# Optimization experiments

Measured on AMD Instinct MI355X. Metric: run time of the kernel, lower is better.

Reference implementation:

```python
import jax, jax.numpy as jnp
import numpy as np
from jax import lax

B, C, D, NH, H, W = 32, 768, 512, 4, 24, 24
HD = C // NH          # 192
FHW = H * W           # 576 (must equal 24*24 per o_proj_img2)


def _p(key, shape, scale=0.02):
    return scale * jax.random.normal(key, shape, dtype=jnp.float32)


def setup_inputs() -> dict:
    ks = jax.random.split(jax.random.key(0), 10)
    return dict(
        img_feats=jax.random.normal(ks[0], (B, C, H, W), jnp.float32),
        txt_feats=jax.random.normal(ks[1], (B, D), jnp.float32),
        fn_w=jnp.ones((C,), jnp.float32), fn_b=jnp.zeros((C,), jnp.float32),
        gn_w=jnp.ones((D,), jnp.float32), gn_b=jnp.zeros((D,), jnp.float32),
        qkv_img_w=_p(ks[2], (3 * C, C)),
        qkv_txt_w=_p(ks[3], (3 * C, D)),
        o_img_w=_p(ks[4], (C, C)), o_img_b=jnp.zeros((C,), jnp.float32),
        o_img2_w=_p(ks[5], (FHW, HD)), o_img2_b=jnp.zeros((FHW,), jnp.float32),
        ffn_norm_w=jnp.ones((C,), jnp.float32), ffn_norm_b=jnp.zeros((C,), jnp.float32),
        fc1_w=_p(ks[6], (C, C)),
        dw_w=_p(ks[7], (C, 1, 3, 3)),
        fc2_w=_p(ks[8], (C, C)),
    )


def layernorm2d(x, w, b, eps=1e-6):
    # normalize over channel dim (dim 1) of NCHW
    u = x.mean(1, keepdims=True)
    s = ((x - u) ** 2).mean(1, keepdims=True)
    x = (x - u) * lax.rsqrt(s + eps)
    return w[:, None, None] * x + b[:, None, None]


def l2norm_last(x, eps=1e-12):
    # F.normalize(x, dim=-1): divide by L2 norm clamped at eps
    n = jnp.sqrt(jnp.sum(x * x, axis=-1, keepdims=True))
    return x / jnp.maximum(n, eps)


def _forward(img_feats, txt_feats, fn_w, fn_b, gn_w, gn_b, qkv_img_w, qkv_txt_w,
             o_img_w, o_img_b, o_img2_w, o_img2_b, ffn_norm_w, ffn_norm_b,
             fc1_w, dw_w, fc2_w):
    x = layernorm2d(img_feats, fn_w, fn_b)
    # guide LayerNorm (torch default eps=1e-5, biased var)
    mu = txt_feats.mean(-1, keepdims=True)
    var = jnp.mean((txt_feats - mu) ** 2, axis=-1, keepdims=True)
    t = (txt_feats - mu) * lax.rsqrt(var + 1e-5) * gn_w + gn_b

    # qkv img: 1x1 conv; channel layout (ng nh hd) -> [B,3,NH,HD,F]
    qkv_img = jnp.einsum('bchw,oc->bohw', x, qkv_img_w).reshape(B, 3, NH, HD, FHW)
    q_img, k_img, v_img = qkv_img[:, 0], qkv_img[:, 1], qkv_img[:, 2]

    # qkv txt: layout 'b (nh (ng hd))' per the two rearranges -> [B,NH,3,HD]
    qkv_txt = (t @ qkv_txt_w.T).reshape(B, NH, 3, HD)
    q_txt, k_txt = qkv_txt[:, :, 0], qkv_txt[:, :, 1]

    # normalize over size-1 trailing dim == x / max(|x|, eps)  (sign-like)
    nq_txt = q_txt / jnp.maximum(jnp.abs(q_txt), 1e-12)          # [B,NH,HD]
    nk_img = l2norm_last(k_img)                                  # [B,NH,HD,F]
    # einsum('bnhd,bnhf->bnhf') with d of size 1 == broadcast multiply over h
    attn1 = jax.nn.softmax(nq_txt[..., None] * nk_img, axis=-1)  # [B,NH,HD,F]
    txt_on_img = jnp.einsum('bnhf,bngf->bnhg', attn1, v_img)     # [B,NH,HD,HD]

    nk_txt = k_txt / jnp.maximum(jnp.abs(k_txt), 1e-12)
    nq_img = l2norm_last(q_img)
    attn2 = jax.nn.softmax(nk_txt[..., None] * nq_img, axis=-1)
    txt_to_img2 = jnp.einsum('bnhf,bngf->bnhg', attn2, v_img)

    img = (txt_on_img + txt_to_img2).reshape(B, NH * HD, HD)     # [B,768,192]
    y = (img @ o_img2_w.T + o_img2_b).reshape(B, C, H, W)        # [B,768,24,24]
    out = jnp.einsum('bchw,oc->bohw', y, o_img_w) + o_img_b[None, :, None, None] + img_feats

    # ConvMlp FFN (mlp_times=1, bias=False convs, exact GELU)
    z = layernorm2d(out, ffn_norm_w, ffn_norm_b)
    z = jnp.einsum('bchw,oc->bohw', z, fc1_w)
    z = lax.conv_general_dilated(z, dw_w, (1, 1), 'SAME',
                                 feature_group_count=C,
                                 dimension_numbers=('NCHW', 'OIHW', 'NCHW'))
    z = jax.nn.gelu(z, approximate=False)
    z = jnp.einsum('bchw,oc->bohw', z, fc2_w)
    return out + z


def reference(img_feats, txt_feats, fn_w, fn_b, gn_w, gn_b, qkv_img_w, qkv_txt_w,
              o_img_w, o_img_b, o_img2_w, o_img2_b, ffn_norm_w, ffn_norm_b,
              fc1_w, dw_w, fc2_w):
    return _forward(img_feats, txt_feats, fn_w, fn_b, gn_w, gn_b, qkv_img_w,
                    qkv_txt_w, o_img_w, o_img_b, o_img2_w, o_img2_b,
                    ffn_norm_w, ffn_norm_b, fc1_w, dw_w, fc2_w)
```

## Files before the change

kernel.cpp:

```cpp
#include <hip/hip_runtime.h>

typedef unsigned short u16;
typedef __attribute__((ext_vector_type(8))) short short8_t;
typedef __attribute__((ext_vector_type(4))) float f32x4;
typedef __attribute__((ext_vector_type(4))) unsigned short u16x4;

static constexpr int cB   = 32;
static constexpr int cC   = 768;
static constexpr int cD   = 512;
static constexpr int cNH  = 4;
static constexpr int cHD  = 192;
static constexpr int cFHW = 576;
static constexpr int cC3  = 2304;

__device__ inline float us2f(u16 s) {
    union { unsigned int u; float f; } v; v.u = ((unsigned int)s) << 16; return v.f;
}
__device__ inline u16 f2bf(float f) {
    union { float f; unsigned int u; } v; v.f = f;
    unsigned int r = v.u + 0x7FFFu + ((v.u >> 16) & 1u);
    return (u16)(r >> 16);
}
__device__ inline float ldflex(const void* p, size_t i, int isf32) {
    return isf32 ? ((const float*)p)[i] : us2f(((const u16*)p)[i]);
}

__device__ inline void gload16(const void* g, void* l) {
    __builtin_amdgcn_global_load_lds(
        (const __attribute__((address_space(1))) void*)g,
        (__attribute__((address_space(3))) void*)l, 16, 0, 0);
}

__global__ void detect_kernel(const u16* __restrict__ raw, int* __restrict__ flags) {
    flags[0] = (raw[0] == 0x3F80u) ? 0 : 1;
}

struct FlatDesc { const void* src[12]; float* dst[12]; int off[13]; };
__global__ __launch_bounds__(256) void flatten_kernel(FlatDesc d, const int* __restrict__ flags) {
    const int isf = flags[0];
    const int gid = blockIdx.x * 256 + threadIdx.x;
    if (gid >= d.off[12]) return;
    int s = 0;
    #pragma unroll
    for (int i = 1; i < 12; i++) s += (gid >= d.off[i]) ? 1 : 0;
    const int j = gid - d.off[s];
    d.dst[s][j] = ldflex(d.src[s], j, isf);
}

__global__ __launch_bounds__(256) void cast_bf16_kernel(
    const void* __restrict__ src, u16* __restrict__ dst, int n, const int* __restrict__ flags)
{
    const int isf = flags[0];
    for (int i = blockIdx.x * 256 + threadIdx.x; i < n; i += gridDim.x * 256)
        dst[i] = isf ? f2bf(((const float*)src)[i]) : ((const u16*)src)[i];
}

__global__ __launch_bounds__(256) void transpose_kernel(
    const void* __restrict__ src, float* __restrict__ dst,
    int Mdim, int Kdim, const int* __restrict__ flags)
{
    __shared__ float t[32][33];
    const int isf = flags[0];
    const int k0 = blockIdx.x * 32, m0 = blockIdx.y * 32;
    const int x = threadIdx.x & 31, y = threadIdx.x >> 5;
    #pragma unroll
    for (int i = 0; i < 4; i++) {
        const int m = y + i * 8;
        t[m][x] = ldflex(src, (size_t)(m0 + m) * Kdim + k0 + x, isf);
    }
    __syncthreads();
    #pragma unroll
    for (int i = 0; i < 4; i++) {
        const int r = y + i * 8;
        dst[(size_t)(k0 + r) * Mdim + m0 + x] = t[x][r];
    }
}

__global__ __launch_bounds__(256) void txt_ln_kernel(
    const float* __restrict__ txt, const float* __restrict__ gw, const float* __restrict__ gb,
    float* __restrict__ tln)
{
    __shared__ float red[8];
    const int b = blockIdx.x, tid = threadIdx.x;
    const float v0 = txt[(size_t)b * cD + tid];
    const float v1 = txt[(size_t)b * cD + 256 + tid];
    float s = v0 + v1, ss = v0 * v0 + v1 * v1;
    #pragma unroll
    for (int o = 1; o < 64; o <<= 1) { s += __shfl_xor(s, o, 64); ss += __shfl_xor(ss, o, 64); }
    const int wid = tid >> 6, lane = tid & 63;
    if (lane == 0) { red[wid] = s; red[4 + wid] = ss; }
    __syncthreads();
    s  = red[0] + red[1] + red[2] + red[3];
    ss = red[4] + red[5] + red[6] + red[7];
    const float mean = s * (1.f / cD);
    const float var  = fmaxf(ss * (1.f / cD) - mean * mean, 0.f);
    const float r = rsqrtf(var + 1e-5f);
    tln[(size_t)b * cD + tid]       = (v0 - mean) * r * gw[tid]       + gb[tid];
    tln[(size_t)b * cD + 256 + tid] = (v1 - mean) * r * gw[tid + 256] + gb[tid + 256];
}

__global__ __launch_bounds__(256) void txt_gemm_kernel(
    const float* __restrict__ Wt, const float* __restrict__ tln, float* __restrict__ out)
{
    const int o  = blockIdx.x * 256 + threadIdx.x;
    const int b0 = blockIdx.y * 8;
    __shared__ float t[8][cD];
    for (int i = threadIdx.x; i < 8 * cD; i += 256)
        t[i >> 9][i & (cD - 1)] = tln[(size_t)(b0 + (i >> 9)) * cD + (i & (cD - 1))];
    __syncthreads();
    float acc[8] = {};
    #pragma unroll 2
    for (int k = 0; k < cD; k += 4) {
        const float w0 = Wt[(size_t)(k + 0) * cC3 + o];
        const float w1 = Wt[(size_t)(k + 1) * cC3 + o];
        const float w2 = Wt[(size_t)(k + 2) * cC3 + o];
        const float w3 = Wt[(size_t)(k + 3) * cC3 + o];
        #pragma unroll
        for (int b = 0; b < 8; b++) {
            const float4 tv = *(const float4*)&t[b][k];
            acc[b] += w0 * tv.x + w1 * tv.y + w2 * tv.z + w3 * tv.w;
        }
    }
    #pragma unroll
    for (int b = 0; b < 8; b++) out[(size_t)(b0 + b) * cC3 + o] = acc[b];
}

template <int RAW>
__global__ __launch_bounds__(1024) void ln_stats_kernel(
    const void* __restrict__ x, size_t xoff, float* __restrict__ mr,
    const int* __restrict__ flags)
{
    const int isf = RAW ? flags[0] : 1;
    const int b = blockIdx.y;
    const int l = threadIdx.x & 63;
    const int f = (blockIdx.x << 6) + l;
    const int cg = threadIdx.x >> 6;
    const size_t base = (size_t)b * cC * cFHW + f;
    const size_t rbase = RAW ? (xoff + base) : base;
    float s = 0.f, ss = 0.f;
    for (int c = cg; c < cC; c += 16) {
        float v = RAW ? ldflex(x, rbase + (size_t)c * cFHW, isf)
                      : ((const float*)x)[base + (size_t)c * cFHW];
        s += v; ss += v * v;
    }
    __shared__ float S[16][64], SS[16][64];
    S[cg][l] = s; SS[cg][l] = ss;
    __syncthreads();
    if (threadIdx.x < 64) {
        float su = 0.f, sq = 0.f;
        #pragma unroll
        for (int i = 0; i < 16; i++) { su += S[i][l]; sq += SS[i][l]; }
        const float mean = su * (1.f / cC);
        const float var  = fmaxf(sq * (1.f / cC) - mean * mean, 0.f);
        float* o = mr + ((size_t)b * cFHW + f) * 2;
        o[0] = mean; o[1] = rsqrtf(var + 1e-6f);
    }
}

template <int XSRC>
__global__ __launch_bounds__(256) void prep_xt_kernel(
    const void* __restrict__ X, size_t xoff, u16* __restrict__ Xt,
    const float* __restrict__ mr, const float* __restrict__ lnw, const float* __restrict__ lnb,
    const int* __restrict__ flags)
{
    __shared__ float t[64][33];
    const int isf = (XSRC == 2) ? flags[0] : 1;
    const int f0 = blockIdx.x * 32, c0 = blockIdx.y * 64, b = blockIdx.z;
    const int tid = threadIdx.x;
    const int fx = tid & 31, cy = tid >> 5;
    const size_t base = (size_t)b * cC * cFHW;
    #pragma unroll
    for (int i = 0; i < 8; i++) {
        const int c = c0 + cy + i * 8;
        const size_t ei = base + (size_t)c * cFHW + f0 + fx;
        t[cy + i * 8][fx] = (XSRC == 2) ? ldflex(X, xoff + ei, isf) : ((const float*)X)[ei];
    }
    __syncthreads();
    const int cx = tid & 31, fy = tid >> 5;
    #pragma unroll
    for (int i = 0; i < 4; i++) {
        const int fl = fy + i * 8;
        const int f = f0 + fl;
        float v0 = t[cx * 2][fl], v1 = t[cx * 2 + 1][fl];
        if (XSRC >= 1) {
            const float* mp = mr + ((size_t)b * cFHW + f) * 2;
            const float mean = mp[0], rst = mp[1];
            v0 = (v0 - mean) * rst * lnw[c0 + cx * 2]     + lnb[c0 + cx * 2];
            v1 = (v1 - mean) * rst * lnw[c0 + cx * 2 + 1] + lnb[c0 + cx * 2 + 1];
        }
        const unsigned int pk = (unsigned int)f2bf(v0) | ((unsigned int)f2bf(v1) << 16);
        *(unsigned int*)(Xt + base + (size_t)f * cC + c0 + cx * 2) = pk;
    }
}

template <int EPI>
__global__ __launch_bounds__(256, 2) void conv_mfma(
    const u16* __restrict__ Wb, const u16* __restrict__ Xt,
    float* __restrict__ outp, const float* __restrict__ bias_m,
    const void* __restrict__ resRaw, size_t resOff, const float* __restrict__ resF,
    u16* __restrict__ vout,
    int M, int K, int Mt, const int* __restrict__ flags)
{
    const int nwg = 9 * Mt;
    int wg = blockIdx.x;
    {
        const int q = nwg >> 3, r = nwg & 7, x = wg & 7, idx = wg >> 3;
        wg = (x < r ? x * (q + 1) : r * (q + 1) + (x - r) * q) + idx;
    }
    const int xt = wg / Mt, yt = wg - xt * Mt;
    const int n0 = xt * 64, m0 = yt * 256, b = blockIdx.z;

    __shared__ __align__(16) u16 A_s[2][256 * 64];
    __shared__ __align__(16) u16 B_s[2][64 * 64];

    const int tid = threadIdx.x;
    const int w = tid >> 6, lane = tid & 63, lq = lane >> 4, lr = lane & 15;
    const int l8 = lane >> 3, c8 = lane & 7;
    const int xch = ((c8 ^ l8) << 4);

    const u16* wbase = Wb + (size_t)m0 * K;
    const u16* xbase = Xt + ((size_t)b * cFHW + n0) * K;

    f32x4 acc[4][4];
    #pragma unroll
    for (int i = 0; i < 4; i++)
        #pragma unroll
        for (int j = 0; j < 4; j++)
            acc[i][j] = (f32x4)0.f;

    const int nt = K >> 6;

    #pragma unroll
    for (int j = 0; j < 8; ++j) {
        const int r = w * 64 + j * 8 + l8;
        gload16((const char*)(wbase + (size_t)r * K) + xch, (char*)&A_s[0][(w * 64 + j * 8) * 64]);
    }
    #pragma unroll
    for (int j = 0; j < 2; ++j) {
        const int r = w * 16 + j * 8 + l8;
        gload16((const char*)(xbase + (size_t)r * K) + xch, (char*)&B_s[0][(w * 16 + j * 8) * 64]);
    }

    int buf = 0;
    #pragma unroll 1
    for (int t = 0; t < nt; ++t) {
        if (t + 1 < nt) {
            const int k0 = (t + 1) << 6;
            #pragma unroll
            for (int j = 0; j < 8; ++j) {
                const int r = w * 64 + j * 8 + l8;
                gload16((const char*)(wbase + (size_t)r * K + k0) + xch,
                        (char*)&A_s[buf ^ 1][(w * 64 + j * 8) * 64]);
            }
            #pragma unroll
            for (int j = 0; j < 2; ++j) {
                const int r = w * 16 + j * 8 + l8;
                gload16((const char*)(xbase + (size_t)r * K + k0) + xch,
                        (char*)&B_s[buf ^ 1][(w * 16 + j * 8) * 64]);
            }
            asm volatile("s_waitcnt vmcnt(10)" ::: "memory");
        } else {
            asm volatile("s_waitcnt vmcnt(0)" ::: "memory");
        }
        __builtin_amdgcn_s_barrier();
        __builtin_amdgcn_sched_barrier(0);
        __builtin_amdgcn_s_setprio(1);
        const u16* As = &A_s[buf][0];
        const u16* Bs = &B_s[buf][0];
        #pragma unroll
        for (int kk = 0; kk < 2; kk++) {
            short8_t af[4], bfr[4];
            #pragma unroll
            for (int fm = 0; fm < 4; fm++) {
                const int ml = w * 64 + fm * 16 + lr;
                af[fm] = *(const short8_t*)((const char*)As + ml * 128 + ((kk * 64 + lq * 16) ^ ((lr & 7) << 4)));
            }
            #pragma unroll
            for (int fn = 0; fn < 4; fn++) {
                const int nl = fn * 16 + lr;
                bfr[fn] = *(const short8_t*)((const char*)Bs + nl * 128 + ((kk * 64 + lq * 16) ^ ((lr & 7) << 4)));
            }
            #pragma unroll
            for (int fm = 0; fm < 4; fm++)
                #pragma unroll
                for (int fn = 0; fn < 4; fn++)
                    acc[fm][fn] = __builtin_amdgcn_mfma_f32_16x16x32_bf16(af[fm], bfr[fn], acc[fm][fn], 0, 0, 0);
        }
        __builtin_amdgcn_s_setprio(0);
        __builtin_amdgcn_s_barrier();
        buf ^= 1;
    }

    const int isf = (EPI == 1) ? flags[0] : 1;
    (void)isf;
    if constexpr (EPI == 3) {
        if (m0 >= 2 * cC) {
            const int mb = m0 - 2 * cC + w * 64;
            #pragma unroll
            for (int fm = 0; fm < 4; fm++)
                #pragma unroll
                for (int fn = 0; fn < 4; fn++)
                    #pragma unroll
                    for (int i = 0; i < 4; i++) {
                        const int mm = mb + fm * 16 + lq * 4 + i;
                        vout[((size_t)b * cC + mm) * cFHW + n0 + fn * 16 + lr] = f2bf(acc[fm][fn][i]);
                    }
        } else {
            #pragma unroll
            for (int fm = 0; fm < 4; fm++)
                #pragma unroll
                for (int fn = 0; fn < 4; fn++)
                    #pragma unroll
                    for (int i = 0; i < 4; i++) {
                        const int mm = m0 + w * 64 + fm * 16 + lq * 4 + i;
                        outp[((size_t)b * 2 * cC + mm) * cFHW + n0 + fn * 16 + lr] = acc[fm][fn][i];
                    }
        }
        return;
    }
    #pragma unroll
    for (int fm = 0; fm < 4; fm++) {
        #pragma unroll
        for (int fn = 0; fn < 4; fn++) {
            #pragma unroll
            for (int i = 0; i < 4; i++) {
                const int mm = m0 + w * 64 + fm * 16 + lq * 4 + i;
                const size_t o = ((size_t)b * M + mm) * cFHW + n0 + fn * 16 + lr;
                float vv = acc[fm][fn][i];
                if constexpr (EPI == 1) {
                    vv += bias_m[mm] + ldflex(resRaw, resOff + o, isf);
                } else if constexpr (EPI == 2) {
                    vv += resF[o];
                }
                outp[o] = vv;
            }
        }
    }
}

__global__ __launch_bounds__(64) void attn_p_kernel(
    const float* __restrict__ qk, const float* __restrict__ tq, u16* __restrict__ Pbf)
{
    const int idx = blockIdx.x;
    const int h = idx % cHD;
    const int bn = idx / cHD;
    const int n = bn & 3, b = bn >> 2;
    const int lane = threadIdx.x;
    const float* qrow = qk + ((size_t)b * 2 * cC + n * cHD + h) * cFHW;
    const float* krow = qk + ((size_t)b * 2 * cC + cC + n * cHD + h) * cFHW;
    float kvr[9], qvr[9];
    #pragma unroll
    for (int j = 0; j < 9; j++) {
        kvr[j] = krow[lane + j * 64];
        qvr[j] = qrow[lane + j * 64];
    }
    float ssk = 0.f, mink = 3.0e38f, maxk = -3.0e38f;
    float ssq = 0.f, minq = 3.0e38f, maxq = -3.0e38f;
    #pragma unroll
    for (int j = 0; j < 9; j++) {
        const float kv = kvr[j]; ssk += kv * kv; maxk = fmaxf(maxk, kv); mink = fminf(mink, kv);
        const float qv = qvr[j]; ssq += qv * qv; maxq = fmaxf(maxq, qv); minq = fminf(minq, qv);
    }
    #pragma unroll
    for (int o = 1; o < 64; o <<= 1) {
        ssk += __shfl_xor(ssk, o, 64); ssq += __shfl_xor(ssq, o, 64);
        maxk = fmaxf(maxk, __shfl_xor(maxk, o, 64)); mink = fminf(mink, __shfl_xor(mink, o, 64));
        maxq = fmaxf(maxq, __shfl_xor(maxq, o, 64)); minq = fminf(minq, __shfl_xor(minq, o, 64));
    }
    const float qt = tq[(size_t)b * cC3 + n * 3 * cHD + h];
    const float kt = tq[(size_t)b * cC3 + n * 3 * cHD + cHD + h];
    const float sign1 = qt / fmaxf(fabsf(qt), 1e-12f);
    const float sign2 = kt / fmaxf(fabsf(kt), 1e-12f);
    const float a1 = sign1 / fmaxf(sqrtf(ssk), 1e-12f);
    const float a2 = sign2 / fmaxf(sqrtf(ssq), 1e-12f);
    const float m1 = fmaxf(a1 * maxk, a1 * mink);
    const float m2 = fmaxf(a2 * maxq, a2 * minq);
    float e1[9], e2[9];
    float z1 = 0.f, z2 = 0.f;
    #pragma unroll
    for (int j = 0; j < 9; j++) {
        e1[j] = expf(a1 * kvr[j] - m1); z1 += e1[j];
        e2[j] = expf(a2 * qvr[j] - m2); z2 += e2[j];
    }
    #pragma unroll
    for (int o = 1; o < 64; o <<= 1) { z1 += __shfl_xor(z1, o, 64); z2 += __shfl_xor(z2, o, 64); }
    const float iz1 = 1.f / z1, iz2 = 1.f / z2;
    u16* prow = Pbf + ((size_t)b * cC + n * cHD + h) * cFHW;
    #pragma unroll
    for (int j = 0; j < 9; j++)
        prow[lane + j * 64] = f2bf(e1[j] * iz1 + e2[j] * iz2);
}

__global__ __launch_bounds__(256, 2) void pv_mfma(
    const u16* __restrict__ P, const u16* __restrict__ V, u16* __restrict__ img, int nbn)
{
    const int nwg = 3 * nbn;
    int wg = blockIdx.x;
    {
        const int q = nwg >> 3, r = nwg & 7, x = wg & 7, idx = wg >> 3;
        wg = (x < r ? x * (q + 1) : r * (q + 1) + (x - r) * q) + idx;
    }
    const int bn = wg / 3, gt = wg - bn * 3;
    const int g0 = gt * 64;
    const int b = bn >> 2, n = bn & 3;

    __shared__ __align__(16) u16 A_s[2][192 * 64];
    __shared__ __align__(16) u16 B_s[2][64 * 64];

    const int tid = threadIdx.x;
    const int w = tid >> 6, lane = tid & 63, lq = lane >> 4, lr = lane & 15;
    const int l8 = lane >> 3, c8 = lane & 7;
    const int xch = ((c8 ^ l8) << 4);

    const u16* pbase = P + ((size_t)b * cC + n * cHD) * cFHW;
    const u16* vbase = V + ((size_t)b * cC + n * cHD + g0) * cFHW;

    f32x4 acc[3][4];
    #pragma unroll
    for (int i = 0; i < 3; i++)
        #pragma unroll
        for (int j = 0; j < 4; j++)
            acc[i][j] = (f32x4)0.f;

    const int nt = cFHW / 64;

    #pragma unroll
    for (int j = 0; j < 6; ++j) {
        const int r = w * 48 + j * 8 + l8;
        gload16((const char*)(pbase + (size_t)r * cFHW) + xch, (char*)&A_s[0][(w * 48 + j * 8) * 64]);
    }
    #pragma unroll
    for (int j = 0; j < 2; ++j) {
        const int r = w * 16 + j * 8 + l8;
        gload16((const char*)(vbase + (size_t)r * cFHW) + xch, (char*)&B_s[0][(w * 16 + j * 8) * 64]);
    }

    int buf = 0;
    #pragma unroll 1
    for (int t = 0; t < nt; ++t) {
        if (t + 1 < nt) {
            const int k0 = (t + 1) << 6;
            #pragma unroll
            for (int j = 0; j < 6; ++j) {
                const int r = w * 48 + j * 8 + l8;
                gload16((const char*)(pbase + (size_t)r * cFHW + k0) + xch,
                        (char*)&A_s[buf ^ 1][(w * 48 + j * 8) * 64]);
            }
            #pragma unroll
            for (int j = 0; j < 2; ++j) {
                const int r = w * 16 + j * 8 + l8;
                gload16((const char*)(vbase + (size_t)r * cFHW + k0) + xch,
                        (char*)&B_s[buf ^ 1][(w * 16 + j * 8) * 64]);
            }
            asm volatile("s_waitcnt vmcnt(8)" ::: "memory");
        } else {
            asm volatile("s_waitcnt vmcnt(0)" ::: "memory");
        }
        __builtin_amdgcn_s_barrier();
        __builtin_amdgcn_sched_barrier(0);
        __builtin_amdgcn_s_setprio(1);
        const u16* As = &A_s[buf][0];
        const u16* Bs = &B_s[buf][0];
        #pragma unroll
        for (int kk = 0; kk < 2; kk++) {
            short8_t af[3], bfr[4];
            #pragma unroll
            for (int fm = 0; fm < 3; fm++) {
                const int ml = w * 48 + fm * 16 + lr;
                af[fm] = *(const short8_t*)((const char*)As + ml * 128 + ((kk * 64 + lq * 16) ^ ((lr & 7) << 4)));
            }
            #pragma unroll
            for (int fn = 0; fn < 4; fn++) {
                const int nl = fn * 16 + lr;
                bfr[fn] = *(const short8_t*)((const char*)Bs + nl * 128 + ((kk * 64 + lq * 16) ^ ((lr & 7) << 4)));
            }
            #pragma unroll
            for (int fm = 0; fm < 3; fm++)
                #pragma unroll
                for (int fn = 0; fn < 4; fn++)
                    acc[fm][fn] = __builtin_amdgcn_mfma_f32_16x16x32_bf16(af[fm], bfr[fn], acc[fm][fn], 0, 0, 0);
        }
        __builtin_amdgcn_s_setprio(0);
        __builtin_amdgcn_s_barrier();
        buf ^= 1;
    }

    #pragma unroll
    for (int fm = 0; fm < 3; fm++)
        #pragma unroll
        for (int fn = 0; fn < 4; fn++)
            #pragma unroll
            for (int i = 0; i < 4; i++) {
                const int mm = w * 48 + fm * 16 + lq * 4 + i;
                img[((size_t)b * cC + n * cHD + mm) * cHD + g0 + fn * 16 + lr] = f2bf(acc[fm][fn][i]);
            }
}

__global__ __launch_bounds__(256, 2) void y_mfma(
    const u16* __restrict__ img, const u16* __restrict__ o2w,
    const float* __restrict__ bias_n, u16* __restrict__ Xt)
{
    const int nwg = 9 * 3;
    int wg = blockIdx.x;
    {
        const int q = nwg >> 3, r = nwg & 7, x = wg & 7, idx = wg >> 3;
        wg = (x < r ? x * (q + 1) : r * (q + 1) + (x - r) * q) + idx;
    }
    const int xt = wg / 3, yt = wg - xt * 3;
    const int n0 = xt * 64, m0 = yt * 256, b = blockIdx.z;
    constexpr int K = cHD;

    __shared__ __align__(16) u16 A_s[2][256 * 64];
    __shared__ __align__(16) u16 B_s[2][64 * 64];

    const int tid = threadIdx.x;
    const int w = tid >> 6, lane = tid & 63, lq = lane >> 4, lr = lane & 15;
    const int l8 = lane >> 3, c8 = lane & 7;
    const int xch = ((c8 ^ l8) << 4);

    const u16* abase = img + ((size_t)b * cC + m0) * K;
    const u16* bbase = o2w + (size_t)n0 * K;

    f32x4 acc[4][4];
    #pragma unroll
    for (int i = 0; i < 4; i++)
        #pragma unroll
        for (int j = 0; j < 4; j++)
            acc[i][j] = (f32x4)0.f;

    const int nt = K >> 6;

    #pragma unroll
    for (int j = 0; j < 8; ++j) {
        const int r = w * 64 + j * 8 + l8;
        gload16((const char*)(abase + (size_t)r * K) + xch, (char*)&A_s[0][(w * 64 + j * 8) * 64]);
    }
    #pragma unroll
    for (int j = 0; j < 2; ++j) {
        const int r = w * 16 + j * 8 + l8;
        gload16((const char*)(bbase + (size_t)r * K) + xch, (char*)&B_s[0][(w * 16 + j * 8) * 64]);
    }

    int buf = 0;
    #pragma unroll 1
    for (int t = 0; t < nt; ++t) {
        if (t + 1 < nt) {
            const int k0 = (t + 1) << 6;
            #pragma unroll
            for (int j = 0; j < 8; ++j) {
                const int r = w * 64 + j * 8 + l8;
                gload16((const char*)(abase + (size_t)r * K + k0) + xch,
                        (char*)&A_s[buf ^ 1][(w * 64 + j * 8) * 64]);
            }
            #pragma unroll
            for (int j = 0; j < 2; ++j) {
                const int r = w * 16 + j * 8 + l8;
                gload16((const char*)(bbase + (size_t)r * K + k0) + xch,
                        (char*)&B_s[buf ^ 1][(w * 16 + j * 8) * 64]);
            }
            asm volatile("s_waitcnt vmcnt(10)" ::: "memory");
        } else {
            asm volatile("s_waitcnt vmcnt(0)" ::: "memory");
        }
        __builtin_amdgcn_s_barrier();
        __builtin_amdgcn_sched_barrier(0);
        __builtin_amdgcn_s_setprio(1);
        const u16* As = &A_s[buf][0];
        const u16* Bs = &B_s[buf][0];
        #pragma unroll
        for (int kk = 0; kk < 2; kk++) {
            short8_t af[4], bfr[4];
            #pragma unroll
            for (int fm = 0; fm < 4; fm++) {
                const int ml = w * 64 + fm * 16 + lr;
                af[fm] = *(const short8_t*)((const char*)As + ml * 128 + ((kk * 64 + lq * 16) ^ ((lr & 7) << 4)));
            }
            #pragma unroll
            for (int fn = 0; fn < 4; fn++) {
                const int nl = fn * 16 + lr;
                bfr[fn] = *(const short8_t*)((const char*)Bs + nl * 128 + ((kk * 64 + lq * 16) ^ ((lr & 7) << 4)));
            }
            #pragma unroll
            for (int fm = 0; fm < 4; fm++)
                #pragma unroll
                for (int fn = 0; fn < 4; fn++)
                    acc[fm][fn] = __builtin_amdgcn_mfma_f32_16x16x32_bf16(af[fm], bfr[fn], acc[fm][fn], 0, 0, 0);
        }
        __builtin_amdgcn_s_setprio(0);
        __builtin_amdgcn_s_barrier();
        buf ^= 1;
    }

    #pragma unroll
    for (int fm = 0; fm < 4; fm++) {
        #pragma unroll
        for (int fn = 0; fn < 4; fn++) {
            const int nn = n0 + fn * 16 + lr;
            const float bn_ = bias_n[nn];
            u16x4 pk;
            #pragma unroll
            for (int i = 0; i < 4; i++) pk[i] = f2bf(acc[fm][fn][i] + bn_);
            const int mm = m0 + w * 64 + fm * 16 + lq * 4;
            *(u16x4*)(Xt + ((size_t)b * cFHW + nn) * cC + mm) = pk;
        }
    }
}

__global__ __launch_bounds__(576) void dwconv_gelu_kernel(
    const float* __restrict__ X, const float* __restrict__ w, float* __restrict__ Y)
{
    const int c = blockIdx.x, b = blockIdx.y;
    __shared__ float t[26][28];
    const int tid = threadIdx.x;
    float* tf = &t[0][0];
    for (int i = tid; i < 26 * 28; i += 576) tf[i] = 0.f;
    __syncthreads();
    const size_t base = ((size_t)b * cC + c) * cFHW;
    const int x = tid % 24, y = tid / 24;
    t[y + 1][x + 1] = X[base + tid];
    __syncthreads();
    float w9[9];
    #pragma unroll
    for (int j = 0; j < 9; j++) w9[j] = w[c * 9 + j];
    float s = 0.f;
    #pragma unroll
    for (int dy = 0; dy < 3; dy++)
        #pragma unroll
        for (int dx = 0; dx < 3; dx++)
            s += w9[dy * 3 + dx] * t[y + dy][x + dx];
    const float g = 0.5f * s * (1.f + erff(s * 0.70710678118654752f));
    Y[base + tid] = g;
}

extern "C" void kernel_launch(void* const* d_in, const int* in_sizes, int n_in,
                              void* d_out, int out_size, void* d_ws, size_t ws_size,
                              hipStream_t stream)
{
    char* p = (char*)d_ws;
    auto allocB = [&](size_t bytes) { char* r = p; p += (bytes + 255) & ~(size_t)255; return r; };
    float* c_txt   = (float*)allocB((size_t)cB * cD * 4);
    float* c_fnw   = (float*)allocB(cC * 4);
    float* c_fnb   = (float*)allocB(cC * 4);
    float* c_gnw   = (float*)allocB(cD * 4);
    float* c_gnb   = (float*)allocB(cD * 4);
    float* c_oib   = (float*)allocB(cC * 4);
    float* c_oi2w  = (float*)allocB((size_t)cFHW * cHD * 4);
    float* c_oi2b  = (float*)allocB(cFHW * 4);
    float* c_ffnw  = (float*)allocB(cC * 4);
    float* c_ffnb  = (float*)allocB(cC * 4);
    float* c_dw    = (float*)allocB(cC * 9 * 4);
    u16*   w_qkv_bf = (u16*)allocB((size_t)cC3 * cC * 2);
    u16*   w_oi_bf  = (u16*)allocB((size_t)cC * cC * 2);
    u16*   w_fc1_bf = (u16*)allocB((size_t)cC * cC * 2);
    u16*   w_fc2_bf = (u16*)allocB((size_t)cC * cC * 2);
    u16*   w_o2w_bf = (u16*)allocB((size_t)cFHW * cHD * 2);
    float* t_qkvtw = (float*)allocB((size_t)cD * cC3 * 4);
    float* tln     = (float*)allocB((size_t)cB * cD * 4);
    int*   flags   = (int*)allocB(256);
    float* tq      = (float*)allocB((size_t)cB * cC3 * 4);
    float* mr1     = (float*)allocB((size_t)cB * cFHW * 2 * 4);
    float* mr2     = (float*)allocB((size_t)cB * cFHW * 2 * 4);
    const size_t fixedBytes = (size_t)(p - (char*)d_ws);
    auto needBytes = [&](int Q) {
        return fixedBytes
             + (size_t)Q * cC * cFHW * 4ull * 2ull
             + (size_t)Q * cC * cHD * 2ull
             + (size_t)Q * cC * cFHW * 2ull
             + (size_t)Q * cC * cFHW * 4ull
             + 8192;
    };
    int Q = 8;
    if (ws_size >= needBytes(32)) Q = 32;
    else if (ws_size >= needBytes(16)) Q = 16;
    const size_t QCF = (size_t)Q * cC * cFHW;
    float* slotA = (float*)allocB(2 * QCF * 4);
    u16*   imgbf = (u16*)allocB((size_t)Q * cC * cHD * 2);
    u16*   XtA   = (u16*)allocB(QCF * 2);
    char*  pvreg = allocB(QCF * 4);
    u16*   Pbf = (u16*)pvreg;
    u16*   Vbf = (u16*)(pvreg + QCF * 2);
    float* A0 = slotA, *A1 = slotA + QCF;
    float* A2 = (float*)pvreg;
    (void)in_sizes; (void)n_in; (void)out_size;

    detect_kernel<<<1, 1, 0, stream>>>((const u16*)d_in[2], flags);

    FlatDesc fd;
    const void* srcs[11] = { d_in[1], d_in[2], d_in[3], d_in[4], d_in[5],
                             d_in[9], d_in[10], d_in[11], d_in[12], d_in[13], d_in[15] };
    float* dsts[11]      = { c_txt, c_fnw, c_fnb, c_gnw, c_gnb,
                             c_oib, c_oi2w, c_oi2b, c_ffnw, c_ffnb, c_dw };
    const int ns[11]     = { cB * cD, cC, cC, cD, cD,
                             cC, cFHW * cHD, cFHW, cC, cC, cC * 9 };
    int tot = 0;
    for (int i = 0; i < 11; i++) { fd.src[i] = srcs[i]; fd.dst[i] = dsts[i]; fd.off[i] = tot; tot += ns[i]; }
    fd.src[11] = srcs[0]; fd.dst[11] = dsts[0];
    fd.off[11] = tot; fd.off[12] = tot;
    flatten_kernel<<<(tot + 255) / 256, 256, 0, stream>>>(fd, flags);

    cast_bf16_kernel<<<512, 256, 0, stream>>>(d_in[6],  w_qkv_bf, cC3 * cC, flags);
    cast_bf16_kernel<<<256, 256, 0, stream>>>(d_in[8],  w_oi_bf,  cC * cC, flags);
    cast_bf16_kernel<<<256, 256, 0, stream>>>(d_in[14], w_fc1_bf, cC * cC, flags);
    cast_bf16_kernel<<<256, 256, 0, stream>>>(d_in[16], w_fc2_bf, cC * cC, flags);
    cast_bf16_kernel<<<128, 256, 0, stream>>>(d_in[10], w_o2w_bf, cFHW * cHD, flags);

    transpose_kernel<<<dim3(cD / 32, cC3 / 32), 256, 0, stream>>>(d_in[7], t_qkvtw, cC3, cD, flags);

    txt_ln_kernel<<<cB, 256, 0, stream>>>(c_txt, c_gnw, c_gnb, tln);
    txt_gemm_kernel<<<dim3(cC3 / 256, cB / 8), 256, 0, stream>>>(t_qkvtw, tln, tq);

    for (int q0 = 0; q0 < cB; q0 += Q) {
        const size_t off = (size_t)q0 * cC * cFHW;
        ln_stats_kernel<1><<<dim3(9, Q), 1024, 0, stream>>>(d_in[0], off, mr1, flags);
        prep_xt_kernel<2><<<dim3(cFHW / 32, cC / 64, Q), 256, 0, stream>>>(
            d_in[0], off, XtA, mr1, c_fnw, c_fnb, flags);
        conv_mfma<3><<<dim3(9 * (cC3 / 256), 1, Q), 256, 0, stream>>>(
            w_qkv_bf, XtA, slotA, nullptr, nullptr, 0, nullptr, Vbf, cC3, cC, cC3 / 256, flags);
        attn_p_kernel<<<Q * cNH * cHD, 64, 0, stream>>>(slotA, tq + (size_t)q0 * cC3, Pbf);
        pv_mfma<<<3 * Q * cNH, 256, 0, stream>>>(Pbf, Vbf, imgbf, Q * cNH);
        y_mfma<<<dim3(27, 1, Q), 256, 0, stream>>>(imgbf, w_o2w_bf, c_oi2b, XtA);
        conv_mfma<1><<<dim3(9 * (cC / 256), 1, Q), 256, 0, stream>>>(
            w_oi_bf, XtA, A0, c_oib, d_in[0], off, nullptr, nullptr, cC, cC, cC / 256, flags);
        ln_stats_kernel<0><<<dim3(9, Q), 1024, 0, stream>>>(A0, 0, mr2, flags);
        prep_xt_kernel<1><<<dim3(cFHW / 32, cC / 64, Q), 256, 0, stream>>>(
            A0, 0, XtA, mr2, c_ffnw, c_ffnb, flags);
        conv_mfma<0><<<dim3(9 * (cC / 256), 1, Q), 256, 0, stream>>>(
            w_fc1_bf, XtA, A2, nullptr, nullptr, 0, nullptr, nullptr, cC, cC, cC / 256, flags);
        dwconv_gelu_kernel<<<dim3(cC, Q), 576, 0, stream>>>(A2, c_dw, A1);
        prep_xt_kernel<0><<<dim3(cFHW / 32, cC / 64, Q), 256, 0, stream>>>(
            A1, 0, XtA, nullptr, nullptr, nullptr, flags);
        conv_mfma<2><<<dim3(9 * (cC / 256), 1, Q), 256, 0, stream>>>(
            w_fc2_bf, XtA, (float*)d_out + off, nullptr, nullptr, 0, A0, nullptr, cC, cC, cC / 256, flags);
    }
}
```

Before: 674.8 us.

## Fold LayerNorm affine into GEMM weights and apply normalization in epilogue

```diff
diff --git a/kernel.cpp b/kernel.cpp
--- a/kernel.cpp
+++ b/kernel.cpp
@@ -53,6 +53,32 @@
     const int isf = flags[0];
     for (int i = blockIdx.x * 256 + threadIdx.x; i < n; i += gridDim.x * 256)
         dst[i] = isf ? f2bf(((const float*)src)[i]) : ((const u16*)src)[i];
+}
+
+__global__ __launch_bounds__(256) void fold_cast_kernel(
+    const void* __restrict__ src, const float* __restrict__ gamma,
+    u16* __restrict__ dst, int n, const int* __restrict__ flags)
+{
+    const int isf = flags[0];
+    for (int i = blockIdx.x * 256 + threadIdx.x; i < n; i += gridDim.x * 256) {
+        const int c = i % cC;
+        dst[i] = f2bf(ldflex(src, i, isf) * gamma[c]);
+    }
+}
+
+__global__ __launch_bounds__(64) void bias_fold_kernel(
+    const void* __restrict__ W, const float* __restrict__ gamma, const float* __restrict__ beta,
+    float* __restrict__ B1, float* __restrict__ B2, const int* __restrict__ flags)
+{
+    const int m = blockIdx.x, lane = threadIdx.x, isf = flags[0];
+    float s1 = 0.f, s2 = 0.f;
+    for (int c = lane; c < cC; c += 64) {
+        const float wv = ldflex(W, (size_t)m * cC + c, isf);
+        s1 += wv * beta[c]; s2 += wv * gamma[c];
+    }
+    #pragma unroll
+    for (int o = 1; o < 64; o <<= 1) { s1 += __shfl_xor(s1, o, 64); s2 += __shfl_xor(s2, o, 64); }
+    if (lane == 0) { B1[m] = s1; B2[m] = s2; }
 }
 
 __global__ __launch_bounds__(256) void transpose_kernel(
@@ -125,42 +151,31 @@
     for (int b = 0; b < 8; b++) out[(size_t)(b0 + b) * cC3 + o] = acc[b];
 }
 
-template <int RAW>
-__global__ __launch_bounds__(1024) void ln_stats_kernel(
-    const void* __restrict__ x, size_t xoff, float* __restrict__ mr,
-    const int* __restrict__ flags)
-{
-    const int isf = RAW ? flags[0] : 1;
-    const int b = blockIdx.y;
-    const int l = threadIdx.x & 63;
-    const int f = (blockIdx.x << 6) + l;
-    const int cg = threadIdx.x >> 6;
-    const size_t base = (size_t)b * cC * cFHW + f;
-    const size_t rbase = RAW ? (xoff + base) : base;
+__global__ __launch_bounds__(256) void ln_stats_rows_kernel(
+    const u16* __restrict__ Xt, float* __restrict__ mr)
+{
+    const int wid = threadIdx.x >> 6, lane = threadIdx.x & 63;
+    const size_t row = (size_t)blockIdx.x * 4 + wid;
+    const u16* r = Xt + row * cC;
     float s = 0.f, ss = 0.f;
-    for (int c = cg; c < cC; c += 16) {
-        float v = RAW ? ldflex(x, rbase + (size_t)c * cFHW, isf)
-                      : ((const float*)x)[base + (size_t)c * cFHW];
-        s += v; ss += v * v;
-    }
-    __shared__ float S[16][64], SS[16][64];
-    S[cg][l] = s; SS[cg][l] = ss;
-    __syncthreads();
-    if (threadIdx.x < 64) {
-        float su = 0.f, sq = 0.f;
-        #pragma unroll
-        for (int i = 0; i < 16; i++) { su += S[i][l]; sq += SS[i][l]; }
-        const float mean = su * (1.f / cC);
-        const float var  = fmaxf(sq * (1.f / cC) - mean * mean, 0.f);
-        float* o = mr + ((size_t)b * cFHW + f) * 2;
-        o[0] = mean; o[1] = rsqrtf(var + 1e-6f);
+    const short8_t a = *(const short8_t*)(r + lane * 8);
+    const u16x4 bq   = *(const u16x4*)(r + 512 + lane * 4);
+    #pragma unroll
+    for (int j = 0; j < 8; j++) { const float v = us2f((u16)a[j]); s += v; ss += v * v; }
+    #pragma unroll
+    for (int j = 0; j < 4; j++) { const float v = us2f(bq[j]); s += v; ss += v * v; }
+    #pragma unroll
+    for (int o = 1; o < 64; o <<= 1) { s += __shfl_xor(s, o, 64); ss += __shfl_xor(ss, o, 64); }
+    if (lane == 0) {
+        const float mean = s * (1.f / cC);
+        const float var  = fmaxf(ss * (1.f / cC) - mean * mean, 0.f);
+        mr[row * 2] = mean; mr[row * 2 + 1] = rsqrtf(var + 1e-6f);
     }
 }
 
 template <int XSRC>
 __global__ __launch_bounds__(256) void prep_xt_kernel(
     const void* __restrict__ X, size_t xoff, u16* __restrict__ Xt,
-    const float* __restrict__ mr, const float* __restrict__ lnw, const float* __restrict__ lnb,
     const int* __restrict__ flags)
 {
     __shared__ float t[64][33];
@@ -181,13 +196,7 @@
     for (int i = 0; i < 4; i++) {
         const int fl = fy + i * 8;
         const int f = f0 + fl;
-        float v0 = t[cx * 2][fl], v1 = t[cx * 2 + 1][fl];
-        if (XSRC >= 1) {
-            const float* mp = mr + ((size_t)b * cFHW + f) * 2;
-            const float mean = mp[0], rst = mp[1];
-            v0 = (v0 - mean) * rst * lnw[c0 + cx * 2]     + lnb[c0 + cx * 2];
-            v1 = (v1 - mean) * rst * lnw[c0 + cx * 2 + 1] + lnb[c0 + cx * 2 + 1];
-        }
+        const float v0 = t[cx * 2][fl], v1 = t[cx * 2 + 1][fl];
         const unsigned int pk = (unsigned int)f2bf(v0) | ((unsigned int)f2bf(v1) << 16);
         *(unsigned int*)(Xt + base + (size_t)f * cC + c0 + cx * 2) = pk;
     }
@@ -199,6 +208,7 @@
     float* __restrict__ outp, const float* __restrict__ bias_m,
     const void* __restrict__ resRaw, size_t resOff, const float* __restrict__ resF,
     u16* __restrict__ vout,
+    const float* __restrict__ aff_mr, const float* __restrict__ aff_B1, const float* __restrict__ aff_B2,
     int M, int K, int Mt, const int* __restrict__ flags)
 {
     const int nwg = 9 * Mt;
@@ -291,30 +301,59 @@
         buf ^= 1;
     }
 
-    const int isf = (EPI == 1) ? flags[0] : 1;
-    (void)isf;
-    if constexpr (EPI == 3) {
-        if (m0 >= 2 * cC) {
-            const int mb = m0 - 2 * cC + w * 64;
+    const int mrow0 = m0 + w * 64;
+
+    if constexpr (EPI == 3 || EPI == 4) {
+        float b1r[4][4], b2r[4][4];
+        #pragma unroll
+        for (int fm = 0; fm < 4; fm++)
+            #pragma unroll
+            for (int i = 0; i < 4; i++) {
+                const int mg = mrow0 + fm * 16 + lq * 4 + i;
+                b1r[fm][i] = aff_B1[mg];
+                b2r[fm][i] = aff_B2[mg];
+            }
+        #pragma unroll
+        for (int fn = 0; fn < 4; fn++) {
+            const int nn = n0 + fn * 16 + lr;
+            const float2 ms = *(const float2*)(aff_mr + ((size_t)b * cFHW + nn) * 2);
+            const float sf = ms.y, mean_sf = ms.x * ms.y;
             #pragma unroll
             for (int fm = 0; fm < 4; fm++)
                 #pragma unroll
-                for (int fn = 0; fn < 4; fn++)
-                    #pragma unroll
-                    for (int i = 0; i < 4; i++) {
-                        const int mm = mb + fm * 16 + lq * 4 + i;
-                        vout[((size_t)b * cC + mm) * cFHW + n0 + fn * 16 + lr] = f2bf(acc[fm][fn][i]);
+                for (int i = 0; i < 4; i++) {
+                    const int mg = mrow0 + fm * 16 + lq * 4 + i;
+                    const float vv = sf * acc[fm][fn][i] + b1r[fm][i] - mean_sf * b2r[fm][i];
+                    if constexpr (EPI == 3) {
+                        if (m0 >= 2 * cC)
+                            vout[((size_t)b * cC + (mg - 2 * cC)) * cFHW + nn] = f2bf(vv);
+                        else
+                            outp[((size_t)b * 2 * cC + mg) * cFHW + nn] = vv;
+                    } else {
+                        outp[((size_t)b * M + mg) * cFHW + nn] = vv;
                     }
-        } else {
-            #pragma unroll
-            for (int fm = 0; fm < 4; fm++)
+                }
+        }
+        return;
+    }
+    if constexpr (EPI == 1) {
+        const int isf = flags[0];
+        #pragma unroll
+        for (int fm = 0; fm < 4; fm++) {
+            #pragma unroll
+            for (int fn = 0; fn < 4; fn++) {
+                const int nn = n0 + fn * 16 + lr;
+                u16x4 pk;
                 #pragma unroll
-                for (int fn = 0; fn < 4; fn++)
-                    #pragma unroll
-                    for (int i = 0; i < 4; i++) {
-                        const int mm = m0 + w * 64 + fm * 16 + lq * 4 + i;
-                        outp[((size_t)b * 2 * cC + mm) * cFHW + n0 + fn * 16 + lr] = acc[fm][fn][i];
-                    }
+                for (int i = 0; i < 4; i++) {
+                    const int mg = mrow0 + fm * 16 + lq * 4 + i;
+                    const size_t o = ((size_t)b * M + mg) * cFHW + nn;
+                    const float vv = acc[fm][fn][i] + bias_m[mg] + ldflex(resRaw, resOff + o, isf);
+                    outp[o] = vv;
+                    pk[i] = f2bf(vv);
+                }
+                *(u16x4*)(vout + ((size_t)b * cFHW + nn) * cC + (mrow0 + fm * 16 + lq * 4)) = pk;
+            }
         }
         return;
     }
@@ -324,14 +363,10 @@
         for (int fn = 0; fn < 4; fn++) {
             #pragma unroll
             for (int i = 0; i < 4; i++) {
-                const int mm = m0 + w * 64 + fm * 16 + lq * 4 + i;
-                const size_t o = ((size_t)b * M + mm) * cFHW + n0 + fn * 16 + lr;
+                const int mg = mrow0 + fm * 16 + lq * 4 + i;
+                const size_t o = ((size_t)b * M + mg) * cFHW + n0 + fn * 16 + lr;
                 float vv = acc[fm][fn][i];
-                if constexpr (EPI == 1) {
-                    vv += bias_m[mm] + ldflex(resRaw, resOff + o, isf);
-                } else if constexpr (EPI == 2) {
-                    vv += resF[o];
-                }
+                if constexpr (EPI == 2) vv += resF[o];
                 outp[o] = vv;
             }
         }
@@ -660,6 +695,10 @@
     float* tq      = (float*)allocB((size_t)cB * cC3 * 4);
     float* mr1     = (float*)allocB((size_t)cB * cFHW * 2 * 4);
     float* mr2     = (float*)allocB((size_t)cB * cFHW * 2 * 4);
+    float* b1q     = (float*)allocB(cC3 * 4);
+    float* b2q     = (float*)allocB(cC3 * 4);
+    float* b1f     = (float*)allocB(cC * 4);
+    float* b2f     = (float*)allocB(cC * 4);
     const size_t fixedBytes = (size_t)(p - (char*)d_ws);
     auto needBytes = [&](int Q) {
         return fixedBytes
@@ -698,38 +737,41 @@
     fd.off[11] = tot; fd.off[12] = tot;
     flatten_kernel<<<(tot + 255) / 256, 256, 0, stream>>>(fd, flags);
 
-    cast_bf16_kernel<<<512, 256, 0, stream>>>(d_in[6],  w_qkv_bf, cC3 * cC, flags);
+    fold_cast_kernel<<<512, 256, 0, stream>>>(d_in[6],  c_fnw,  w_qkv_bf, cC3 * cC, flags);
     cast_bf16_kernel<<<256, 256, 0, stream>>>(d_in[8],  w_oi_bf,  cC * cC, flags);
-    cast_bf16_kernel<<<256, 256, 0, stream>>>(d_in[14], w_fc1_bf, cC * cC, flags);
+    fold_cast_kernel<<<256, 256, 0, stream>>>(d_in[14], c_ffnw, w_fc1_bf, cC * cC, flags);
     cast_bf16_kernel<<<256, 256, 0, stream>>>(d_in[16], w_fc2_bf, cC * cC, flags);
     cast_bf16_kernel<<<128, 256, 0, stream>>>(d_in[10], w_o2w_bf, cFHW * cHD, flags);
 
+    bias_fold_kernel<<<cC3, 64, 0, stream>>>(d_in[6],  c_fnw,  c_fnb,  b1q, b2q, flags);
+    bias_fold_kernel<<<cC,  64, 0, stream>>>(d_in[14], c_ffnw, c_ffnb, b1f, b2f, flags);
+
     transpose_kernel<<<dim3(cD / 32, cC3 / 32), 256, 0, stream>>>(d_in[7], t_qkvtw, cC3, cD, flags);
-
     txt_ln_kernel<<<cB, 256, 0, stream>>>(c_txt, c_gnw, c_gnb, tln);
     txt_gemm_kernel<<<dim3(cC3 / 256, cB / 8), 256, 0, stream>>>(t_qkvtw, tln, tq);
 
     for (int q0 = 0; q0 < cB; q0 += Q) {
         const size_t off = (size_t)q0 * cC * cFHW;
-        ln_stats_kernel<1><<<dim3(9, Q), 1024, 0, stream>>>(d_in[0], off, mr1, flags);
-        prep_xt_kernel<2><<<dim3(cFHW / 32, cC / 64, Q), 256, 0, stream>>>(
-            d_in[0], off, XtA, mr1, c_fnw, c_fnb, flags);
+        u16* XtB = (u16*)((float*)d_out + off);
+        prep_xt_kernel<2><<<dim3(cFHW / 32, cC / 64, Q), 256, 0, stream>>>(d_in[0], off, XtA, flags);
+        ln_stats_rows_kernel<<<Q * cFHW / 4, 256, 0, stream>>>(XtA, mr1);
         conv_mfma<3><<<dim3(9 * (cC3 / 256), 1, Q), 256, 0, stream>>>(
-            w_qkv_bf, XtA, slotA, nullptr, nullptr, 0, nullptr, Vbf, cC3, cC, cC3 / 256, flags);
+            w_qkv_bf, XtA, slotA, nullptr, nullptr, 0, nullptr, Vbf,
+            mr1, b1q, b2q, cC3, cC, cC3 / 256, flags);
         attn_p_kernel<<<Q * cNH * cHD, 64, 0, stream>>>(slotA, tq + (size_t)q0 * cC3, Pbf);
         pv_mfma<<<3 * Q * cNH, 256, 0, stream>>>(Pbf, Vbf, imgbf, Q * cNH);
         y_mfma<<<dim3(27, 1, Q), 256, 0, stream>>>(imgbf, w_o2w_bf, c_oi2b, XtA);
         conv_mfma<1><<<dim3(9 * (cC / 256), 1, Q), 256, 0, stream>>>(
-            w_oi_bf, XtA, A0, c_oib, d_in[0], off, nullptr, nullptr, cC, cC, cC / 256, flags);
-        ln_stats_kernel<0><<<dim3(9, Q), 1024, 0, stream>>>(A0, 0, mr2, flags);
-        prep_xt_kernel<1><<<dim3(cFHW / 32, cC / 64, Q), 256, 0, stream>>>(
-            A0, 0, XtA, mr2, c_ffnw, c_ffnb, flags);
-        conv_mfma<0><<<dim3(9 * (cC / 256), 1, Q), 256, 0, stream>>>(
-            w_fc1_bf, XtA, A2, nullptr, nullptr, 0, nullptr, nullptr, cC, cC, cC / 256, flags);
+            w_oi_bf, XtA, A0, c_oib, d_in[0], off, nullptr, XtB,
+            nullptr, nullptr, nullptr, cC, cC, cC / 256, flags);
+        ln_stats_rows_kernel<<<Q * cFHW / 4, 256, 0, stream>>>(XtB, mr2);
+        conv_mfma<4><<<dim3(9 * (cC / 256), 1, Q), 256, 0, stream>>>(
+            w_fc1_bf, XtB, A2, nullptr, nullptr, 0, nullptr, nullptr,
+            mr2, b1f, b2f, cC, cC, cC / 256, flags);
         dwconv_gelu_kernel<<<dim3(cC, Q), 576, 0, stream>>>(A2, c_dw, A1);
-        prep_xt_kernel<0><<<dim3(cFHW / 32, cC / 64, Q), 256, 0, stream>>>(
-            A1, 0, XtA, nullptr, nullptr, nullptr, flags);
+        prep_xt_kernel<0><<<dim3(cFHW / 32, cC / 64, Q), 256, 0, stream>>>(A1, 0, XtA, flags);
         conv_mfma<2><<<dim3(9 * (cC / 256), 1, Q), 256, 0, stream>>>(
-            w_fc2_bf, XtA, (float*)d_out + off, nullptr, nullptr, 0, A0, nullptr, cC, cC, cC / 256, flags);
-    }
-}
+            w_fc2_bf, XtA, (float*)d_out + off, nullptr, nullptr, 0, A0, nullptr,
+            nullptr, nullptr, nullptr, cC, cC, cC / 256, flags);
+    }
+}
```

Measured after the change: 689.9 us. 2.2% more time.
